# Kernel optimization log

Measured on AMD Instinct MI355X. Metric: run time of the kernel, lower is better.

## Reference

```python
import jax, jax.numpy as jnp
import numpy as np

T, B, D, H = 64, 512, 768, 12
HD = D // H
EPS = 1e-8  # torch cosine_similarity eps


def setup_inputs() -> dict:
    key = jax.random.key(0)
    k0, k1, k2, k3 = jax.random.split(key, 4)
    node_embs = jax.random.normal(k0, (T, B, D), dtype=jnp.float32)
    in_proj_w = jax.random.normal(k1, (3 * D, D), dtype=jnp.float32) * 0.02
    in_proj_b = jnp.zeros((3 * D,), dtype=jnp.float32)
    out_proj_w = jax.random.normal(k2, (D, D), dtype=jnp.float32) * 0.02
    out_proj_b = jnp.zeros((D,), dtype=jnp.float32)
    return {"node_embs": node_embs, "in_proj_w": in_proj_w, "in_proj_b": in_proj_b,
            "out_proj_w": out_proj_w, "out_proj_b": out_proj_b}


def reference(node_embs, in_proj_w, in_proj_b, out_proj_w, out_proj_b):
    # node_embs: (T, B, D). Original loops over t calling MHA on (B, 1, D)
    # i.e. self-attention across the B axis with batch=1, fused here over T.
    qkv = jnp.einsum('tbd,ed->tbe', node_embs, in_proj_w) + in_proj_b  # (T, B, 3D)
    q, k, v = jnp.split(qkv, 3, axis=-1)

    def heads(x):  # (T, B, D) -> (T, H, B, HD)
        return x.reshape(T, B, H, HD).transpose(0, 2, 1, 3)

    q, k, v = heads(q), heads(k), heads(v)
    scores = jnp.einsum('thqd,thkd->thqk', q, k) / np.sqrt(HD).astype(np.float32)
    attn = jax.nn.softmax(scores, axis=-1)
    ctx = jnp.einsum('thqk,thkd->thqd', attn, v)  # (T, H, B, HD)
    ctx = ctx.transpose(0, 2, 1, 3).reshape(T, B, D)
    out = jnp.einsum('tbd,ed->tbe', ctx, out_proj_w) + out_proj_b  # (T, B, D)

    # cosine similarity between all pairs over B, then mean over first index
    norm = jnp.maximum(jnp.linalg.norm(out, axis=-1), EPS)  # (T, B)
    xn = out / norm[..., None]
    sim = jnp.einsum('tid,tjd->tij', xn, xn)  # (T, B, B)
    adj = sim.mean(axis=1)[..., None]  # (T, B, 1) == (T, B, N) with N=1
    return adj
```

## Files before the change

kernel.cpp:

```cpp
#include <hip/hip_runtime.h>

#define T_ 64
#define B_ 512
#define D_ 768
#define H_ 12
#define HD_ 64
#define M1 (T_*B_)
#define N_QKV (3*D_)

typedef __attribute__((ext_vector_type(8))) short short8;
typedef __attribute__((ext_vector_type(4))) float f32x4;

__device__ __forceinline__ unsigned short f2b(float f) {
  unsigned int u = __float_as_uint(f);
  u = (u + 0x7FFFu + ((u >> 16) & 1u)) >> 16;
  return (unsigned short)u;
}
__device__ __forceinline__ float b2f(unsigned short s) {
  return __uint_as_float(((unsigned int)s) << 16);
}

__device__ __forceinline__ void load_lds16(const unsigned short* g, unsigned short* l) {
  __builtin_amdgcn_global_load_lds(
      (const __attribute__((address_space(1))) unsigned int*)g,
      (__attribute__((address_space(3))) unsigned int*)l, 16, 0, 0);
}

__global__ __launch_bounds__(256) void k_cast(const float* __restrict__ in,
                                              unsigned short* __restrict__ out, int n4) {
  int i = blockIdx.x * blockDim.x + threadIdx.x;
  if (i < n4) {
    float4 v = ((const float4*)in)[i];
    ushort4 o;
    o.x = f2b(v.x); o.y = f2b(v.y); o.z = f2b(v.z); o.w = f2b(v.w);
    ((ushort4*)out)[i] = o;
  }
}


#define GEMM_BODY(Aptr, Bptr, Sbuf) \
  unsigned short* As = Sbuf; \
  unsigned short* Bs = Sbuf + 8192; \
  const int tid = threadIdx.x; \
  const int m0 = blockIdx.y * 128, n0 = blockIdx.x * 128; \
  const int lane = tid & 63, wave = tid >> 6; \
  const int ln = lane & 15, quad = lane >> 4; \
  const int wm = (wave & 1) * 64, wn = (wave >> 1) * 64; \
  f32x4 acc[4][4] = {}; \
  for (int k0 = 0; k0 < 768; k0 += 64) { \
    __syncthreads(); \
    _Pragma("unroll") \
    for (int it = 0; it < 4; it++) { \
      int s = wave*256 + it*64 + lane; \
      int r = s >> 3, cp = s & 7, c = cp ^ (r & 7); \
      load_lds16(&Aptr[(size_t)(m0+r)*768 + k0 + c*8], &As[s*8]); \
      load_lds16(&Bptr[(size_t)(n0+r)*768 + k0 + c*8], &Bs[s*8]); \
    } \
    __syncthreads(); \
    _Pragma("unroll") \
    for (int j = 0; j < 2; j++) { \
      short8 a[4], b[4]; \
      _Pragma("unroll") \
      for (int i = 0; i < 4; i++) { \
        int row = wm + i*16 + ln; \
        int cp = (j*4 + quad) ^ (row & 7); \
        a[i] = *(const short8*)&As[row*64 + cp*8]; \
      } \
      _Pragma("unroll") \
      for (int i = 0; i < 4; i++) { \
        int row = wn + i*16 + ln; \
        int cp = (j*4 + quad) ^ (row & 7); \
        b[i] = *(const short8*)&Bs[row*64 + cp*8]; \
      } \
      _Pragma("unroll") \
      for (int mi = 0; mi < 4; mi++) \
        _Pragma("unroll") \
        for (int ni = 0; ni < 4; ni++) \
          acc[mi][ni] = __builtin_amdgcn_mfma_f32_16x16x32_bf16(a[mi], b[ni], acc[mi][ni], 0, 0, 0); \
    } \
  }

__global__ __launch_bounds__(256) void k_gemm_qkv(
    const unsigned short* __restrict__ A,
    const unsigned short* __restrict__ Bw,
    const float* __restrict__ bias,
    unsigned short* __restrict__ qo,
    unsigned short* __restrict__ ko,
    unsigned short* __restrict__ vTo)
{
  __shared__ __align__(16) unsigned short Sbuf[128*136];
  GEMM_BODY(A, Bw, Sbuf)

  if (n0 >= 1536) {
    __syncthreads();
#pragma unroll
    for (int mi = 0; mi < 4; mi++)
#pragma unroll
      for (int ni = 0; ni < 4; ni++) {
        int col = wn + ni*16 + ln;
        int row = wm + mi*16 + quad*4;
        float bi = bias[n0 + col];
        ushort4 pk;
        pk.x = f2b(acc[mi][ni][0] + bi);
        pk.y = f2b(acc[mi][ni][1] + bi);
        pk.z = f2b(acc[mi][ni][2] + bi);
        pk.w = f2b(acc[mi][ni][3] + bi);
        *(ushort4*)&Sbuf[col*136 + row] = pk;
      }
    __syncthreads();
    {
      int col = tid >> 1, half = tid & 1;
      int cg = n0 + col - 1536;
      int h = cg >> 6, hd = cg & 63;
      int t = m0 >> 9;
      int bb0 = (m0 & 511) + half*64;
      size_t o = ((size_t)(t*H_ + h)*HD_ + hd)*B_ + bb0;
#pragma unroll
      for (int j = 0; j < 8; j++)
        *(uint4*)&vTo[o + j*8] = *(const uint4*)&Sbuf[col*136 + half*64 + j*8];
    }
  } else {
    unsigned short* dst = (n0 < 768) ? qo : ko;
    int colbase = (n0 < 768) ? n0 : (n0 - 768);
#pragma unroll
    for (int mi = 0; mi < 4; mi++)
#pragma unroll
      for (int ni = 0; ni < 4; ni++)
#pragma unroll
        for (int r = 0; r < 4; r++) {
          int row = m0 + wm + mi*16 + quad*4 + r;
          int within = colbase + wn + ni*16 + ln;
          float val = acc[mi][ni][r] + bias[(n0 < 768 ? 0 : 768) + within];
          int t = row >> 9, bb = row & 511;
          int h = within >> 6, hd = within & 63;
          dst[((size_t)(t*H_ + h)*B_ + bb)*HD_ + hd] = f2b(val);
        }
  }
}

__global__ __launch_bounds__(256) void k_gemm_out(
    const unsigned short* __restrict__ A,
    const unsigned short* __restrict__ Bw,
    const float* __restrict__ bias,
    float* __restrict__ out)
{
  __shared__ __align__(16) unsigned short Sbuf[2*128*64];
  GEMM_BODY(A, Bw, Sbuf)
#pragma unroll
  for (int mi = 0; mi < 4; mi++)
#pragma unroll
    for (int ni = 0; ni < 4; ni++)
#pragma unroll
      for (int r = 0; r < 4; r++) {
        int row = m0 + wm + mi*16 + quad*4 + r;
        int col = n0 + wn + ni*16 + ln;
        out[(size_t)row*768 + col] = acc[mi][ni][r] + bias[col];
      }
}

__global__ __launch_bounds__(256) void k_attn(
    const unsigned short* __restrict__ q,
    const unsigned short* __restrict__ k,
    const unsigned short* __restrict__ vT,
    unsigned short* __restrict__ ctx)
{
  __shared__ __align__(16) unsigned short Ks[64*64];
  __shared__ __align__(16) unsigned short VT[64*64];
  __shared__ __align__(16) unsigned short Ps[4*16*72];
  const int tid = threadIdx.x;
  const int lane = tid & 63, wave = tid >> 6;
  const int ln = lane & 15, quad = lane >> 4;
  const int th = blockIdx.y;
  const int t = th / H_, h = th - t*H_;
  const int q0 = blockIdx.x * 64;
  const size_t base  = (size_t)th * (B_*HD_);
  const size_t baseT = (size_t)th * (HD_*B_);

  short8 qf0, qf1;
  {
    const unsigned short* qp = &q[base + (size_t)(q0 + wave*16 + ln)*HD_ + quad*8];
    qf0 = *(const short8*)qp;
    qf1 = *(const short8*)(qp + 32);
  }
  f32x4 acc[4] = {};
  float dpart[4] = {0.f,0.f,0.f,0.f};
  unsigned short* Pw = &Ps[wave*16*72];

  for (int kt = 0; kt < B_; kt += 64) {
    __syncthreads();
#pragma unroll
    for (int it = 0; it < 2; it++) {
      int s = it*256 + tid;
      int r = s >> 3, cp = s & 7, c = cp ^ (r & 7);
      load_lds16(&k[base + (size_t)(kt + r)*HD_ + c*8], &Ks[s*8]);
      load_lds16(&vT[baseT + (size_t)r*B_ + kt + c*8], &VT[s*8]);
    }
    __syncthreads();
    f32x4 sf[4] = {};
#pragma unroll
    for (int i = 0; i < 4; i++) {
      int row = i*16 + ln;
      short8 b0 = *(const short8*)&Ks[row*64 + (quad     ^ (row & 7))*8];
      short8 b1 = *(const short8*)&Ks[row*64 + ((4+quad) ^ (row & 7))*8];
      sf[i] = __builtin_amdgcn_mfma_f32_16x16x32_bf16(qf0, b0, sf[i], 0, 0, 0);
      sf[i] = __builtin_amdgcn_mfma_f32_16x16x32_bf16(qf1, b1, sf[i], 0, 0, 0);
    }
#pragma unroll
    for (int i = 0; i < 4; i++) {
      int colbase = (i*16 + ln) ^ (quad*16);
#pragma unroll
      for (int r = 0; r < 4; r++) {
        float p = __expf(sf[i][r] * 0.125f);
        dpart[r] += p;
        Pw[(quad*4 + r)*72 + colbase] = f2b(p);
      }
    }
    short8 pa0, pa1;
    {
      int c0 = (quad*8) ^ (16*(ln >> 2));
      int c1 = (quad*8 + 32) ^ (16*(ln >> 2));
      pa0 = *(const short8*)&Pw[ln*72 + c0];
      pa1 = *(const short8*)&Pw[ln*72 + c1];
    }
#pragma unroll
    for (int s = 0; s < 4; s++) {
      int row = s*16 + ln;
      short8 vb0 = *(const short8*)&VT[row*64 + (quad     ^ (row & 7))*8];
      short8 vb1 = *(const short8*)&VT[row*64 + ((4+quad) ^ (row & 7))*8];
      acc[s] = __builtin_amdgcn_mfma_f32_16x16x32_bf16(pa0, vb0, acc[s], 0, 0, 0);
      acc[s] = __builtin_amdgcn_mfma_f32_16x16x32_bf16(pa1, vb1, acc[s], 0, 0, 0);
    }
  }
#pragma unroll
  for (int r = 0; r < 4; r++) {
    float d = dpart[r];
    d += __shfl_xor(d, 1); d += __shfl_xor(d, 2);
    d += __shfl_xor(d, 4); d += __shfl_xor(d, 8);
    dpart[r] = 1.f / d;
  }
  int qrow = q0 + wave*16 + quad*4;
#pragma unroll
  for (int r = 0; r < 4; r++) {
    size_t o = ((size_t)t*B_ + (qrow + r))*D_ + h*HD_ + ln;
#pragma unroll
    for (int s = 0; s < 4; s++)
      ctx[o + s*16] = f2b(acc[s][r] * dpart[r]);
  }
}

__global__ __launch_bounds__(256) void k_norms1(const float* __restrict__ out,
                                                float* __restrict__ norms,
                                                float* __restrict__ pmvec)
{
  __shared__ float wsum[4*768];
  int blk = blockIdx.x;
  int t = blk >> 3, c = blk & 7;
  int wave = threadIdx.x >> 6, lane = threadIdx.x & 63;
  float macc[12];
#pragma unroll
  for (int j = 0; j < 12; j++) macc[j] = 0.f;
  for (int i = 0; i < 16; i++) {
    int b = c*64 + wave*16 + i;
    const float* row = &out[((size_t)t*B_ + b)*D_];
    float x[12]; float ss = 0.f;
#pragma unroll
    for (int j = 0; j < 12; j++) { x[j] = row[lane + 64*j]; ss += x[j]*x[j]; }
#pragma unroll
    for (int off = 32; off; off >>= 1) ss += __shfl_xor(ss, off);
    float nr = fmaxf(sqrtf(ss), 1e-8f);
    if (lane == 0) norms[(size_t)t*B_ + b] = nr;
    float inv = 1.f / nr;
#pragma unroll
    for (int j = 0; j < 12; j++) macc[j] += x[j]*inv;
  }
#pragma unroll
  for (int j = 0; j < 12; j++) wsum[wave*768 + 64*j + lane] = macc[j];
  __syncthreads();
  for (int d = threadIdx.x; d < 768; d += 256) {
    pmvec[(size_t)blk*768 + d] = wsum[d] + wsum[768 + d] + wsum[1536 + d] + wsum[2304 + d];
  }
}

__global__ __launch_bounds__(256) void k_norms2(const float* __restrict__ pmvec,
                                                float* __restrict__ mvec)
{
  int t = blockIdx.x;
  for (int d = threadIdx.x; d < 768; d += 256) {
    float s = 0.f;
#pragma unroll
    for (int c = 0; c < 8; c++) s += pmvec[(size_t)(t*8 + c)*768 + d];
    mvec[t*768 + d] = s * (1.0f/512.0f);
  }
}

__global__ __launch_bounds__(256) void k_adj(const float* __restrict__ out,
                                             const float* __restrict__ norms,
                                             const float* __restrict__ mvec,
                                             float* __restrict__ adj)
{
  int idx = blockIdx.x*4 + (threadIdx.x >> 6);
  int lane = threadIdx.x & 63;
  int t = idx >> 9;
  const float* row = &out[(size_t)idx*768];
  const float* m = &mvec[t*768];
  float dot = 0.f;
#pragma unroll
  for (int j = 0; j < 12; j++) dot += row[lane + 64*j] * m[lane + 64*j];
#pragma unroll
  for (int off = 32; off; off >>= 1) dot += __shfl_xor(dot, off);
  if (lane == 0) adj[idx] = dot / norms[idx];
}

extern "C" void kernel_launch(void* const* d_in, const int* in_sizes, int n_in,
                              void* d_out, int out_size, void* d_ws, size_t ws_size,
                              hipStream_t stream)
{
  const float* node = (const float*)d_in[0];
  const float* wqkv = (const float*)d_in[1];
  const float* bqkv = (const float*)d_in[2];
  const float* wout = (const float*)d_in[3];
  const float* bout = (const float*)d_in[4];
  float* adj = (float*)d_out;

  char* ws = (char*)d_ws;
  const size_t SZ = (size_t)M1*D_*2;
  unsigned short* q_bf    = (unsigned short*)(ws);
  unsigned short* k_bf    = (unsigned short*)(ws + SZ);
  unsigned short* vT_bf   = (unsigned short*)(ws + 2*SZ);
  unsigned short* ctx_bf  = (unsigned short*)(ws + 3*SZ);
  unsigned short* x_bf    = (unsigned short*)(ws + 4*SZ);
  unsigned short* wqkv_bf = (unsigned short*)(ws + 5*SZ);
  unsigned short* wout_bf = (unsigned short*)(ws + 5*SZ + 3538944);
  float* out_f            = (float*)(ws);
  float* pmvec            = (float*)(ws + 4*SZ);
  float* norms            = (float*)(ws + 5*SZ + 3538944 + 1179648);
  float* mvec             = (float*)(ws + 5*SZ + 3538944 + 1179648 + 131072);

  k_cast<<<24576, 256, 0, stream>>>(node, x_bf, (M1*D_)/4);
  k_cast<<<1728, 256, 0, stream>>>(wqkv, wqkv_bf, (N_QKV*D_)/4);
  k_cast<<<576, 256, 0, stream>>>(wout, wout_bf, (D_*D_)/4);
  k_gemm_qkv<<<dim3(N_QKV/128, M1/128), 256, 0, stream>>>(x_bf, wqkv_bf, bqkv, q_bf, k_bf, vT_bf);
  k_attn<<<dim3(B_/64, T_*H_), 256, 0, stream>>>(q_bf, k_bf, vT_bf, ctx_bf);
  k_gemm_out<<<dim3(D_/128, M1/128), 256, 0, stream>>>(ctx_bf, wout_bf, bout, out_f);
  k_norms1<<<T_*8, 256, 0, stream>>>(out_f, norms, pmvec);
  k_norms2<<<T_, 256, 0, stream>>>(pmvec, mvec);
  k_adj<<<M1/4, 256, 0, stream>>>(out_f, norms, mvec, adj);
}
```

Before: 538.2 us.

## Fuse casts, remap blocks per XCD, widen attention blocks, store output as bf16

Merges the three fp32-to-bf16 cast launches into one kernel. Remaps the GEMM and attention grids to 1D so that blocks sharing rows land on the same XCD, aiming for better L2 reuse. Attention blocks grow to 512 threads covering 128 queries, so each K/V tile loaded into LDS serves twice as many queries. The out-projection result is stored as bf16 instead of fp32, halving traffic for the norm and adjacency passes at some cost in precision.

```diff
diff --git a/kernel.cpp b/kernel.cpp
--- a/kernel.cpp
+++ b/kernel.cpp
@@ -26,15 +26,22 @@
       (__attribute__((address_space(3))) unsigned int*)l, 16, 0, 0);
 }
 
-__global__ __launch_bounds__(256) void k_cast(const float* __restrict__ in,
-                                              unsigned short* __restrict__ out, int n4) {
-  int i = blockIdx.x * blockDim.x + threadIdx.x;
-  if (i < n4) {
-    float4 v = ((const float4*)in)[i];
-    ushort4 o;
-    o.x = f2b(v.x); o.y = f2b(v.y); o.z = f2b(v.z); o.w = f2b(v.w);
-    ((ushort4*)out)[i] = o;
-  }
+#define N4_NODE 6291456
+#define N4_WQKV 442368
+#define N4_WOUT 147456
+__global__ __launch_bounds__(256) void k_cast_all(
+    const float* __restrict__ node, const float* __restrict__ wqkv,
+    const float* __restrict__ wout, unsigned short* __restrict__ x_bf,
+    unsigned short* __restrict__ wqkv_bf, unsigned short* __restrict__ wout_bf) {
+  int i = blockIdx.x * 256 + threadIdx.x;
+  const float* src; unsigned short* dst; int off;
+  if (i < N4_NODE)                 { src = node; dst = x_bf;    off = i; }
+  else if (i < N4_NODE + N4_WQKV)  { src = wqkv; dst = wqkv_bf; off = i - N4_NODE; }
+  else                             { src = wout; dst = wout_bf; off = i - N4_NODE - N4_WQKV; }
+  float4 v = ((const float4*)src)[off];
+  ushort4 o;
+  o.x = f2b(v.x); o.y = f2b(v.y); o.z = f2b(v.z); o.w = f2b(v.w);
+  ((ushort4*)dst)[off] = o;
 }
 
 
@@ -42,7 +49,6 @@
   unsigned short* As = Sbuf; \
   unsigned short* Bs = Sbuf + 8192; \
   const int tid = threadIdx.x; \
-  const int m0 = blockIdx.y * 128, n0 = blockIdx.x * 128; \
   const int lane = tid & 63, wave = tid >> 6; \
   const int ln = lane & 15, quad = lane >> 4; \
   const int wm = (wave & 1) * 64, wn = (wave >> 1) * 64; \
@@ -89,6 +95,10 @@
     unsigned short* __restrict__ vTo)
 {
   __shared__ __align__(16) unsigned short Sbuf[128*136];
+  const int bb = blockIdx.x;
+  const int xcd = bb & 7, idx = bb >> 3;
+  const int m0 = (xcd*32 + idx/18) * 128;
+  const int n0 = (idx%18) * 128;
   GEMM_BODY(A, Bw, Sbuf)
 
   if (n0 >= 1536) {
@@ -131,9 +141,9 @@
           int row = m0 + wm + mi*16 + quad*4 + r;
           int within = colbase + wn + ni*16 + ln;
           float val = acc[mi][ni][r] + bias[(n0 < 768 ? 0 : 768) + within];
-          int t = row >> 9, bb = row & 511;
+          int t = row >> 9, bbv = row & 511;
           int h = within >> 6, hd = within & 63;
-          dst[((size_t)(t*H_ + h)*B_ + bb)*HD_ + hd] = f2b(val);
+          dst[((size_t)(t*H_ + h)*B_ + bbv)*HD_ + hd] = f2b(val);
         }
   }
 }
@@ -142,9 +152,13 @@
     const unsigned short* __restrict__ A,
     const unsigned short* __restrict__ Bw,
     const float* __restrict__ bias,
-    float* __restrict__ out)
+    unsigned short* __restrict__ outb)
 {
   __shared__ __align__(16) unsigned short Sbuf[2*128*64];
+  const int bb = blockIdx.x;
+  const int xcd = bb & 7, idx = bb >> 3;
+  const int m0 = (xcd*32 + idx/6) * 128;
+  const int n0 = (idx%6) * 128;
   GEMM_BODY(A, Bw, Sbuf)
 #pragma unroll
   for (int mi = 0; mi < 4; mi++)
@@ -154,11 +168,11 @@
       for (int r = 0; r < 4; r++) {
         int row = m0 + wm + mi*16 + quad*4 + r;
         int col = n0 + wn + ni*16 + ln;
-        out[(size_t)row*768 + col] = acc[mi][ni][r] + bias[col];
+        outb[(size_t)row*768 + col] = f2b(acc[mi][ni][r] + bias[col]);
       }
 }
 
-__global__ __launch_bounds__(256) void k_attn(
+__global__ __launch_bounds__(512) void k_attn(
     const unsigned short* __restrict__ q,
     const unsigned short* __restrict__ k,
     const unsigned short* __restrict__ vT,
@@ -166,13 +180,15 @@
 {
   __shared__ __align__(16) unsigned short Ks[64*64];
   __shared__ __align__(16) unsigned short VT[64*64];
-  __shared__ __align__(16) unsigned short Ps[4*16*72];
+  __shared__ __align__(16) unsigned short Ps[8*16*72];
   const int tid = threadIdx.x;
   const int lane = tid & 63, wave = tid >> 6;
   const int ln = lane & 15, quad = lane >> 4;
-  const int th = blockIdx.y;
+  const int bb = blockIdx.x;
+  const int xcd = bb & 7, idx = bb >> 3;
+  const int th = xcd*96 + (idx >> 2);
+  const int q0 = (idx & 3) * 128;
   const int t = th / H_, h = th - t*H_;
-  const int q0 = blockIdx.x * 64;
   const size_t base  = (size_t)th * (B_*HD_);
   const size_t baseT = (size_t)th * (HD_*B_);
 
@@ -188,9 +204,8 @@
 
   for (int kt = 0; kt < B_; kt += 64) {
     __syncthreads();
-#pragma unroll
-    for (int it = 0; it < 2; it++) {
-      int s = it*256 + tid;
+    {
+      int s = tid;
       int r = s >> 3, cp = s & 7, c = cp ^ (r & 7);
       load_lds16(&k[base + (size_t)(kt + r)*HD_ + c*8], &Ks[s*8]);
       load_lds16(&vT[baseT + (size_t)r*B_ + kt + c*8], &VT[s*8]);
@@ -248,7 +263,7 @@
   }
 }
 
-__global__ __launch_bounds__(256) void k_norms1(const float* __restrict__ out,
+__global__ __launch_bounds__(256) void k_norms1(const unsigned short* __restrict__ outb,
                                                 float* __restrict__ norms,
                                                 float* __restrict__ pmvec)
 {
@@ -261,10 +276,10 @@
   for (int j = 0; j < 12; j++) macc[j] = 0.f;
   for (int i = 0; i < 16; i++) {
     int b = c*64 + wave*16 + i;
-    const float* row = &out[((size_t)t*B_ + b)*D_];
+    const unsigned short* row = &outb[((size_t)t*B_ + b)*D_];
     float x[12]; float ss = 0.f;
 #pragma unroll
-    for (int j = 0; j < 12; j++) { x[j] = row[lane + 64*j]; ss += x[j]*x[j]; }
+    for (int j = 0; j < 12; j++) { x[j] = b2f(row[lane + 64*j]); ss += x[j]*x[j]; }
 #pragma unroll
     for (int off = 32; off; off >>= 1) ss += __shfl_xor(ss, off);
     float nr = fmaxf(sqrtf(ss), 1e-8f);
@@ -293,7 +308,7 @@
   }
 }
 
-__global__ __launch_bounds__(256) void k_adj(const float* __restrict__ out,
+__global__ __launch_bounds__(256) void k_adj(const unsigned short* __restrict__ outb,
                                              const float* __restrict__ norms,
                                              const float* __restrict__ mvec,
                                              float* __restrict__ adj)
@@ -301,11 +316,11 @@
   int idx = blockIdx.x*4 + (threadIdx.x >> 6);
   int lane = threadIdx.x & 63;
   int t = idx >> 9;
-  const float* row = &out[(size_t)idx*768];
+  const unsigned short* row = &outb[(size_t)idx*768];
   const float* m = &mvec[t*768];
   float dot = 0.f;
 #pragma unroll
-  for (int j = 0; j < 12; j++) dot += row[lane + 64*j] * m[lane + 64*j];
+  for (int j = 0; j < 12; j++) dot += b2f(row[lane + 64*j]) * m[lane + 64*j];
 #pragma unroll
   for (int off = 32; off; off >>= 1) dot += __shfl_xor(dot, off);
   if (lane == 0) adj[idx] = dot / norms[idx];
@@ -331,18 +346,16 @@
   unsigned short* x_bf    = (unsigned short*)(ws + 4*SZ);
   unsigned short* wqkv_bf = (unsigned short*)(ws + 5*SZ);
   unsigned short* wout_bf = (unsigned short*)(ws + 5*SZ + 3538944);
-  float* out_f            = (float*)(ws);
+  unsigned short* out_bf  = (unsigned short*)(ws);
   float* pmvec            = (float*)(ws + 4*SZ);
   float* norms            = (float*)(ws + 5*SZ + 3538944 + 1179648);
   float* mvec             = (float*)(ws + 5*SZ + 3538944 + 1179648 + 131072);
 
-  k_cast<<<24576, 256, 0, stream>>>(node, x_bf, (M1*D_)/4);
-  k_cast<<<1728, 256, 0, stream>>>(wqkv, wqkv_bf, (N_QKV*D_)/4);
-  k_cast<<<576, 256, 0, stream>>>(wout, wout_bf, (D_*D_)/4);
-  k_gemm_qkv<<<dim3(N_QKV/128, M1/128), 256, 0, stream>>>(x_bf, wqkv_bf, bqkv, q_bf, k_bf, vT_bf);
-  k_attn<<<dim3(B_/64, T_*H_), 256, 0, stream>>>(q_bf, k_bf, vT_bf, ctx_bf);
-  k_gemm_out<<<dim3(D_/128, M1/128), 256, 0, stream>>>(ctx_bf, wout_bf, bout, out_f);
-  k_norms1<<<T_*8, 256, 0, stream>>>(out_f, norms, pmvec);
+  k_cast_all<<<26880, 256, 0, stream>>>(node, wqkv, wout, x_bf, wqkv_bf, wout_bf);
+  k_gemm_qkv<<<4608, 256, 0, stream>>>(x_bf, wqkv_bf, bqkv, q_bf, k_bf, vT_bf);
+  k_attn<<<3072, 512, 0, stream>>>(q_bf, k_bf, vT_bf, ctx_bf);
+  k_gemm_out<<<1536, 256, 0, stream>>>(ctx_bf, wout_bf, bout, out_bf);
+  k_norms1<<<T_*8, 256, 0, stream>>>(out_bf, norms, pmvec);
   k_norms2<<<T_, 256, 0, stream>>>(pmvec, mvec);
-  k_adj<<<M1/4, 256, 0, stream>>>(out_f, norms, mvec, adj);
-}
+  k_adj<<<M1/4, 256, 0, stream>>>(out_bf, norms, mvec, adj);
+}
```

Result: faster. 463.9 us (-13.8%).
